# Performance work log

Hardware: AMD Instinct MI355X
Metric: run time of the kernel (lower is better)

## Reference

```python
import jax, jax.numpy as jnp
import numpy as np

# Module hyperparameters (init_kwargs)
IN_CHANNELS = 16
N_SEGMENTS = 32
LOGSIG_DEPTH = 2  # depth-2 log-signature: level1 increments + Levy areas
LOGSIG_CHANNELS = IN_CHANNELS + IN_CHANNELS * (IN_CHANNELS - 1) // 2  # 136

N_BATCHS = 8
BATCH_SIZE = 16
NT = 2048


def setup_inputs() -> dict:
    key = jax.random.key(0)
    k1, k2 = jax.random.split(key)
    inp = jax.random.normal(k1, (N_BATCHS * BATCH_SIZE, NT, IN_CHANNELS), dtype=jnp.float32)
    # lengths >= 2*n_segments so the repeat-padding branch of the torch code is never taken
    length = jax.random.randint(k2, (N_BATCHS,), 256, NT + 1)
    return {"inp": inp, "length": length, "n_batchs": N_BATCHS}


def _gather_time(arr, idx):
    # arr: [B, nT, ...], idx: [B, K] -> [B, K, ...]
    B, nT = arr.shape[0], arr.shape[1]
    trail = arr.shape[2:]
    flat = arr.reshape(B, nT, -1)
    idx_b = jnp.broadcast_to(idx[:, :, None], (B, idx.shape[1], flat.shape[-1]))
    out = jnp.take_along_axis(flat, idx_b, axis=1)
    return out.reshape(B, idx.shape[1], *trail)


def reference(inp, length, n_batchs):
    # Depth-2 log-signature over N_SEGMENTS variable-length windows per group.
    # Level 1: window increment x_b - x_a.
    # Level 2 (Lyndon words i<j): Levy area A_ij = 0.5 * sum_{l in [a,b)} [(x_l - x_a)_i dx_l_j - (x_l - x_a)_j dx_l_i]
    # computed from a prefix sum P_t = sum_{l<t} (x_l ^ dx_l) gathered at segment boundaries.
    B, nT, d = inp.shape
    batch_size = B // n_batchs
    S = N_SEGMENTS

    dx = inp[:, 1:] - inp[:, :-1]                              # [B, nT-1, d]
    c = jnp.einsum('bti,btj->btij', inp[:, :-1], dx)
    c = c - jnp.swapaxes(c, -1, -2)                            # antisymmetric outer products
    P = jnp.concatenate(
        [jnp.zeros((B, 1, d, d), inp.dtype), jnp.cumsum(c, axis=1)], axis=1
    )                                                          # [B, nT, d, d], P_t = sum_{l<t} c_l

    # boundary point indices per group: t_vec = round(linspace(1, L, S+1)), 0-based
    frac = jnp.arange(S + 1, dtype=jnp.float32) / S
    Lf = length.astype(jnp.float32)[:, None]
    tv = jnp.round(1.0 + (Lf - 1.0) * frac[None, :]).astype(jnp.int32) - 1  # [n_batchs, S+1]
    idx = jnp.repeat(tv, batch_size, axis=0)                   # [B, S+1]

    xb = _gather_time(inp, idx)                                # [B, S+1, d]
    Pb = _gather_time(P, idx)                                  # [B, S+1, d, d]

    xa, xe = xb[:, :-1], xb[:, 1:]
    lvl1 = xe - xa                                             # [B, S, d]
    corr = jnp.einsum('bsi,bsj->bsij', xa, lvl1)
    corr = corr - jnp.swapaxes(corr, -1, -2)
    A = 0.5 * (Pb[:, 1:] - Pb[:, :-1] - corr)                  # [B, S, d, d] Levy areas
    iu, ju = jnp.triu_indices(d, k=1)
    lvl2 = A[:, :, iu, ju]                                     # [B, S, d(d-1)/2]
    return jnp.concatenate([lvl1, lvl2], axis=-1)              # [B, S, LOGSIG_CHANNELS]
```

## Files before the change

kernel.cpp:

```cpp
#include <hip/hip_runtime.h>

#define NT    2048
#define D     16
#define NSEG  32
#define NPAIR 120
#define NOUTC 136
#define CHUNK 64

__global__ __launch_bounds__(128) void logsig_kernel(
    const float* __restrict__ inp,
    const int*   __restrict__ length,
    float*       __restrict__ out,
    int batch_size)
{
    const int blk = blockIdx.x;
    const int b   = blk / NSEG;
    const int s   = blk % NSEG;
    const int g   = b / batch_size;
    const int tid = threadIdx.x;

    const float Lm1 = __fadd_rn((float)length[g], -1.0f);
    const float f0  = (float)s       * (1.0f / 32.0f);
    const float f1  = (float)(s + 1) * (1.0f / 32.0f);
    const int t0 = (int)rintf(__fadd_rn(1.0f, __fmul_rn(Lm1, f0))) - 1;
    const int t1 = (int)rintf(__fadd_rn(1.0f, __fmul_rn(Lm1, f1))) - 1;

    const float* xrow = inp + (size_t)b * NT * D;

    __shared__ float4 xs4[(CHUNK + 1) * (D / 4)];
    float* xs = (float*)xs4;
    __shared__ float xa_s[D], xe_s[D];

    int pi, pj;
    {
        int p = tid, i = 0;
        while (i < D - 1 && p >= (D - 1 - i)) { p -= (D - 1 - i); ++i; }
        pi = i; pj = i + 1 + p;
    }

    if (tid < D) {
        xa_s[tid] = xrow[(size_t)t0 * D + tid];
        xe_s[tid] = xrow[(size_t)t1 * D + tid];
    }
    __syncthreads();

    float acc = 0.0f;
    for (int tc = t0; tc < t1; tc += CHUNK) {
        const int len  = min(CHUNK, t1 - tc);
        const int nvec = (len + 1) * (D / 4);
        const float4* src = (const float4*)(xrow + (size_t)tc * D);
        __syncthreads();
        for (int v = tid; v < nvec; v += 128)
            xs4[v] = src[v];
        __syncthreads();
        if (tid < NPAIR) {
            float xi = xs[pi];
            float xj = xs[pj];
            for (int t = 0; t < len; ++t) {
                const float xi2 = xs[(t + 1) * D + pi];
                const float xj2 = xs[(t + 1) * D + pj];
                acc = fmaf(xi,  xj2 - xj, acc);
                acc = fmaf(-xj, xi2 - xi, acc);
                xi = xi2; xj = xj2;
            }
        }
    }

    const size_t obase = ((size_t)b * NSEG + s) * NOUTC;
    if (tid < D) {
        out[obase + tid] = xe_s[tid] - xa_s[tid];
    }
    if (tid < NPAIR) {
        const float xai = xa_s[pi], xaj = xa_s[pj];
        const float l1i = xe_s[pi] - xai;
        const float l1j = xe_s[pj] - xaj;
        const float corr = xai * l1j - xaj * l1i;
        out[obase + D + tid] = 0.5f * (acc - corr);
    }
}

extern "C" void kernel_launch(void* const* d_in, const int* in_sizes, int n_in,
                              void* d_out, int out_size, void* d_ws, size_t ws_size,
                              hipStream_t stream)
{
    const float* inp    = (const float*)d_in[0];
    const int*   length = (const int*)d_in[1];
    float*       out    = (float*)d_out;

    const int B  = in_sizes[0] / (NT * D);
    const int G  = in_sizes[1];
    const int bs = B / G;

    const int grid = B * NSEG;
    logsig_kernel<<<grid, 128, 0, stream>>>(inp, length, out, bs);
}
```

Measured before the change: 11.59 us.

## Compute segment Levy areas with split-bf16 MFMA instead of per-pair scalar loops

Replaces the per-pair scalar accumulation over time with a 16x16 matrix product x^T·dx per segment, computed on MFMA units. It uses three bf16 products (hi·hi, hi·lo, lo·hi) to approximate fp32 accuracy. The segment is loaded once, transposed into shared memory, and the antisymmetric part is formed from the accumulator and its transpose. Blocks shrink to one 64-lane wave. The kernel now assumes a segment spans at most 64 steps, which holds for NT=2048 and 32 segments. The split-bf16 scheme adds a small rounding difference compared with plain fp32.

Result: faster. 9.929 us (-14.4%).

```diff
diff --git a/kernel.cpp b/kernel.cpp
--- a/kernel.cpp
+++ b/kernel.cpp
@@ -3,79 +3,104 @@
 #define NT    2048
 #define D     16
 #define NSEG  32
-#define NPAIR 120
 #define NOUTC 136
-#define CHUNK 64
 
-__global__ __launch_bounds__(128) void logsig_kernel(
+typedef __attribute__((ext_vector_type(8))) short bf16x8;
+typedef __attribute__((ext_vector_type(4))) float f32x4;
+
+__global__ __launch_bounds__(64) void logsig_kernel(
     const float* __restrict__ inp,
     const int*   __restrict__ length,
     float*       __restrict__ out,
     int batch_size)
 {
-    const int blk = blockIdx.x;
-    const int b   = blk / NSEG;
-    const int s   = blk % NSEG;
-    const int g   = b / batch_size;
-    const int tid = threadIdx.x;
+    const int blk  = blockIdx.x;
+    const int b    = blk / NSEG;
+    const int s    = blk % NSEG;
+    const int g    = b / batch_size;
+    const int lane = threadIdx.x;
+
+    __shared__ float xT[D * 68];
+    __shared__ float Cs[16 * 17];
 
     const float Lm1 = __fadd_rn((float)length[g], -1.0f);
-    const float f0  = (float)s       * (1.0f / 32.0f);
-    const float f1  = (float)(s + 1) * (1.0f / 32.0f);
-    const int t0 = (int)rintf(__fadd_rn(1.0f, __fmul_rn(Lm1, f0))) - 1;
-    const int t1 = (int)rintf(__fadd_rn(1.0f, __fmul_rn(Lm1, f1))) - 1;
+    const int t0 = (int)rintf(__fadd_rn(1.0f, __fmul_rn(Lm1, (float)s       * (1.0f/32.0f)))) - 1;
+    const int t1 = (int)rintf(__fadd_rn(1.0f, __fmul_rn(Lm1, (float)(s + 1) * (1.0f/32.0f)))) - 1;
+    const int n  = t1 - t0;
 
     const float* xrow = inp + (size_t)b * NT * D;
+    const float4* src = (const float4*)(xrow + (size_t)t0 * D);
 
-    __shared__ float4 xs4[(CHUNK + 1) * (D / 4)];
-    float* xs = (float*)xs4;
-    __shared__ float xa_s[D], xe_s[D];
-
-    int pi, pj;
-    {
-        int p = tid, i = 0;
-        while (i < D - 1 && p >= (D - 1 - i)) { p -= (D - 1 - i); ++i; }
-        pi = i; pj = i + 1 + p;
-    }
-
-    if (tid < D) {
-        xa_s[tid] = xrow[(size_t)t0 * D + tid];
-        xe_s[tid] = xrow[(size_t)t1 * D + tid];
+    const int nvec = (n + 1) * 4;
+    for (int v = lane; v < nvec; v += 64) {
+        const float4 q = src[v];
+        const int t  = v >> 2;
+        const int c4 = (v & 3) << 2;
+        xT[(c4 + 0) * 68 + t] = q.x;
+        xT[(c4 + 1) * 68 + t] = q.y;
+        xT[(c4 + 2) * 68 + t] = q.z;
+        xT[(c4 + 3) * 68 + t] = q.w;
     }
     __syncthreads();
 
-    float acc = 0.0f;
-    for (int tc = t0; tc < t1; tc += CHUNK) {
-        const int len  = min(CHUNK, t1 - tc);
-        const int nvec = (len + 1) * (D / 4);
-        const float4* src = (const float4*)(xrow + (size_t)tc * D);
-        __syncthreads();
-        for (int v = tid; v < nvec; v += 128)
-            xs4[v] = src[v];
-        __syncthreads();
-        if (tid < NPAIR) {
-            float xi = xs[pi];
-            float xj = xs[pj];
-            for (int t = 0; t < len; ++t) {
-                const float xi2 = xs[(t + 1) * D + pi];
-                const float xj2 = xs[(t + 1) * D + pj];
-                acc = fmaf(xi,  xj2 - xj, acc);
-                acc = fmaf(-xj, xi2 - xi, acc);
-                xi = xi2; xj = xj2;
-            }
+    const int ch = lane & 15;
+    const int tb = lane >> 4;
+    const float* base = &xT[ch * 68];
+
+    f32x4 acc = {0.f, 0.f, 0.f, 0.f};
+    const int nchunks = (n > 32) ? 2 : 1;
+
+    for (int c = 0; c < nchunks; ++c) {
+        const int kb = c * 32 + 8 * tb;
+        const f32x4 q0 = *(const f32x4*)(base + kb);
+        const f32x4 q1 = *(const f32x4*)(base + kb + 4);
+        const float x9 = base[kb + 8];
+        float xv[9] = {q0[0], q0[1], q0[2], q0[3], q1[0], q1[1], q1[2], q1[3], x9};
+
+        bf16x8 Ah, Al, Bh, Bl;
+        #pragma unroll
+        for (int e = 0; e < 8; ++e) {
+            const int idx = kb + e;
+            const float xm  = (idx <= n) ? xv[e] : 0.0f;
+            const float dxm = (idx <  n) ? (xv[e + 1] - xv[e]) : 0.0f;
+            const unsigned bx = __float_as_uint(xm);
+            Ah[e] = (short)(bx >> 16);
+            const float lx = xm - __uint_as_float(bx & 0xFFFF0000u);
+            Al[e] = (short)(__float_as_uint(lx) >> 16);
+            const unsigned bd = __float_as_uint(dxm);
+            Bh[e] = (short)(bd >> 16);
+            const float ld = dxm - __uint_as_float(bd & 0xFFFF0000u);
+            Bl[e] = (short)(__float_as_uint(ld) >> 16);
         }
+        acc = __builtin_amdgcn_mfma_f32_16x16x32_bf16(Ah, Bh, acc, 0, 0, 0);
+        acc = __builtin_amdgcn_mfma_f32_16x16x32_bf16(Ah, Bl, acc, 0, 0, 0);
+        acc = __builtin_amdgcn_mfma_f32_16x16x32_bf16(Al, Bh, acc, 0, 0, 0);
     }
 
+    #pragma unroll
+    for (int e = 0; e < 4; ++e)
+        Cs[(4 * tb + e) * 17 + ch] = acc[e];
+    __syncthreads();
+
+    const float xa_j = base[0];
+    const float xe_j = base[n];
     const size_t obase = ((size_t)b * NSEG + s) * NOUTC;
-    if (tid < D) {
-        out[obase + tid] = xe_s[tid] - xa_s[tid];
+
+    if (tb == 0) {
+        out[obase + ch] = xe_j - xa_j;
     }
-    if (tid < NPAIR) {
-        const float xai = xa_s[pi], xaj = xa_s[pj];
-        const float l1i = xe_s[pi] - xai;
-        const float l1j = xe_s[pj] - xaj;
-        const float corr = xai * l1j - xaj * l1i;
-        out[obase + D + tid] = 0.5f * (acc - corr);
+    #pragma unroll
+    for (int e = 0; e < 4; ++e) {
+        const int i = 4 * tb + e;
+        const int j = ch;
+        if (i < j) {
+            const float Mt   = Cs[j * 17 + i];
+            const float xa_i = xT[i * 68 + 0];
+            const float xe_i = xT[i * 68 + n];
+            const float corr = xa_i * (xe_j - xa_j) - xa_j * (xe_i - xa_i);
+            const int oidx   = 15 * i - (i * (i - 1)) / 2 + (j - i - 1);
+            out[obase + D + oidx] = 0.5f * (acc[e] - Mt - corr);
+        }
     }
 }
 
@@ -92,5 +117,5 @@
     const int bs = B / G;
 
     const int grid = B * NSEG;
-    logsig_kernel<<<grid, 128, 0, stream>>>(inp, length, out, bs);
+    logsig_kernel<<<grid, 64, 0, stream>>>(inp, length, out, bs);
 }
```
